# Performance work log

Hardware: AMD Instinct MI355X
Metric: run time of the kernel (lower is better)

The kernel has to match this reference:

```python
import jax, jax.numpy as jnp
import numpy as np

KS = 3          # deformable kernel size
PAD = 1         # padding (kernel_size // 2)
EPS = 1e-5      # BatchNorm eps


def conv2d(x, w, b):
    # plain 3x3 conv, stride 1, pad 1, NCHW / OIHW
    y = jax.lax.conv_general_dilated(x, w, window_strides=(1, 1),
                                     padding=[(PAD, PAD), (PAD, PAD)],
                                     dimension_numbers=("NCHW", "OIHW", "NCHW"))
    return y + b[None, :, None, None]


def deform_conv(x, offset, mask, w, b):
    # modulated deformable conv v2 (torchvision deform_conv2d semantics)
    B, C, H, W = x.shape
    K = KS * KS
    ky, kx = jnp.meshgrid(jnp.arange(KS), jnp.arange(KS), indexing="ij")
    ky = ky.reshape(-1).astype(x.dtype)
    kx = kx.reshape(-1).astype(x.dtype)
    off = offset.reshape(B, K, 2, H, W)          # channel order: (dy, dx) per kernel tap
    dy, dx = off[:, :, 0], off[:, :, 1]          # [B,K,H,W]
    py = dy + (ky - PAD)[None, :, None, None] + jnp.arange(H, dtype=x.dtype)[None, None, :, None]
    px = dx + (kx - PAD)[None, :, None, None] + jnp.arange(W, dtype=x.dtype)[None, None, None, :]
    y0 = jnp.floor(py); x0 = jnp.floor(px)
    ly = py - y0; lx = px - x0
    y0i = y0.astype(jnp.int32); x0i = x0.astype(jnp.int32)
    y1i = y0i + 1; x1i = x0i + 1
    xf = x.reshape(B, C, H * W)

    def gather(yi, xi):
        valid = (yi >= 0) & (yi < H) & (xi >= 0) & (xi < W)          # zero padding outside
        idx = jnp.clip(yi, 0, H - 1) * W + jnp.clip(xi, 0, W - 1)    # [B,K,H,W]
        g = jax.vmap(lambda xb, ib: jnp.take(xb, ib, axis=1))(xf, idx.reshape(B, -1))
        g = g.reshape(B, C, K, H, W)
        return g * valid[:, None].astype(x.dtype)

    v = (gather(y0i, x0i) * ((1 - ly) * (1 - lx))[:, None]
         + gather(y0i, x1i) * ((1 - ly) * lx)[:, None]
         + gather(y1i, x0i) * (ly * (1 - lx))[:, None]
         + gather(y1i, x1i) * (ly * lx)[:, None])                    # [B,C,K,H,W]
    v = v * mask[:, None]                                            # modulation
    out = jnp.einsum("bckhw,ock->bohw", v, w.reshape(w.shape[0], C, K))
    return out + b[None, :, None, None]


def setup_inputs() -> dict:
    key = jax.random.key(0)
    ks = jax.random.split(key, 5)
    B, Cin, Cout, H, W = 8, 64, 64, 128, 128
    K = KS * KS
    x = jax.random.normal(ks[0], (B, Cin, H, W), jnp.float32)
    off_w = jax.random.normal(ks[1], (2 * K, Cin, KS, KS), jnp.float32) * 0.01
    off_b = jnp.zeros((2 * K,), jnp.float32)
    mod_w = jax.random.normal(ks[2], (K, Cin, KS, KS), jnp.float32) * 0.01
    mod_b = jnp.zeros((K,), jnp.float32)
    w = jax.random.normal(ks[3], (Cout, Cin, KS, KS), jnp.float32) * (1.0 / np.sqrt(Cin * K))
    b = jnp.zeros((Cout,), jnp.float32)
    gamma = jnp.ones((Cout,), jnp.float32)
    beta = jnp.zeros((Cout,), jnp.float32)
    return {"x": x, "off_w": off_w, "off_b": off_b, "mod_w": mod_w,
            "mod_b": mod_b, "w": w, "b": b, "gamma": gamma, "beta": beta}


def reference(x, off_w, off_b, mod_w, mod_b, w, b, gamma, beta):
    offset = conv2d(x, off_w, off_b)                       # [B,2K,H,W]
    mask = 2.0 * jax.nn.sigmoid(conv2d(x, mod_w, mod_b))   # [B,K,H,W]
    y = deform_conv(x, offset, mask, w, b)                 # [B,Cout,H,W]
    # BatchNorm2d (training-mode batch stats, biased variance)
    mean = y.mean(axis=(0, 2, 3), keepdims=True)
    var = y.var(axis=(0, 2, 3), keepdims=True)
    yn = (y - mean) / jnp.sqrt(var + EPS)
    yn = gamma[None, :, None, None] * yn + beta[None, :, None, None]
    return jax.nn.relu(yn)
```

## Files before the change

### kernel.cpp

```cpp
#include <hip/hip_runtime.h>
#include <math.h>

#define Hn 128
#define Wn 128
#define HW 16384
#define NPIX 131072
#define EPSv 1e-5f

#define XT_OFF   0
#define WBTA_OFF 4194304
#define WBTB_OFF 4204544
#define STAT_OFF 4225024


typedef short s16x8 __attribute__((ext_vector_type(8)));
typedef unsigned short u16x4 __attribute__((ext_vector_type(4)));
typedef float f32x4 __attribute__((ext_vector_type(4)));
typedef unsigned int u32x4 __attribute__((ext_vector_type(4)));

__device__ __forceinline__ unsigned short f2bf(float f) {
  unsigned u = __float_as_uint(f);
  return (unsigned short)((u + 0x7fffu + ((u >> 16) & 1u)) >> 16);
}
__device__ __forceinline__ float bf2f(unsigned short s) {
  return __uint_as_float((unsigned)s << 16);
}
__device__ __forceinline__ unsigned cvt_pk_bf16(float lo, float hi) {
  unsigned r;
  asm("v_cvt_pk_bf16_f32 %0, %1, %2" : "=v"(r) : "v"(lo), "v"(hi));
  return r;
}

__global__ __launch_bounds__(256) void prep_kernel(
    const float* __restrict__ off_w, const float* __restrict__ mod_w,
    const float* __restrict__ w, unsigned short* __restrict__ wbtA,
    unsigned short* __restrict__ wbtB, float* __restrict__ stat) {
  int i = blockIdx.x * 256 + threadIdx.x;
  if (i < 128) stat[i] = 0.f;
  if (i < 20480) {
    int e = i & 31, oc = (i >> 5) & 31, it = i >> 10;
    int tp = it % 5, chunk = it / 5;
    int tap = tp * 2 + (e >> 4);
    int c = (chunk << 4) + (e & 15);
    float v = 0.f;
    if (tap < 9) {
      if (oc < 18) v = off_w[(oc * 64 + c) * 9 + tap];
      else if (oc < 27) v = mod_w[((oc - 18) * 64 + c) * 9 + tap];
    }
    wbtA[i] = f2bf(v);
  } else if (i < 20480 + 40960) {
    int j = i - 20480;
    int j3 = j & 7;
    int l = (j >> 3) & 63;
    int nt = (j >> 9) & 3;
    int it = j >> 11;
    int tp = it % 5, chunk = it / 5;
    int tap = tp * 2 + (l >> 5);
    int c = (chunk << 4) + (((l >> 4) & 1) << 3) + j3;
    int oc = (nt << 4) + (l & 15);
    float v = (tap < 9) ? w[(oc * 64 + c) * 9 + tap] : 0.f;
    wbtB[j] = f2bf(v);
  }
}

__global__ __launch_bounds__(256) void xform_kernel(
    const float* __restrict__ x, unsigned short* __restrict__ xt) {
  int blk = blockIdx.x;
  int b = blk & 7;
  int hw = ((blk >> 3) << 8) + threadIdx.x;
  const float* xb = x + ((size_t)(b << 6) << 14) + hw;
  unsigned short* o = xt + (((size_t)(b << 14)) + hw) * 64;
#pragma unroll
  for (int g = 0; g < 8; ++g) {
    float v[8];
#pragma unroll
    for (int j = 0; j < 8; ++j) v[j] = xb[(size_t)((g << 3) + j) << 14];
    s16x8 pk;
#pragma unroll
    for (int j = 0; j < 8; ++j) pk[j] = (short)f2bf(v[j]);
    *(s16x8*)(o + (g << 3)) = pk;
  }
}

__global__ __launch_bounds__(256, 4) void fused_dconv_kernel(
    const unsigned short* __restrict__ xt, const unsigned short* __restrict__ wbtA,
    const unsigned short* __restrict__ wbtB,
    const float* __restrict__ off_b, const float* __restrict__ mod_b,
    const float* __restrict__ bias, float* __restrict__ y) {
  __shared__ float offm[27 * 128];
  __shared__ unsigned short geow[9 * 128 * 4];
  __shared__ unsigned short geoi[9 * 128];
  int t = threadIdx.x;
  int bx = blockIdx.x;
  int b = bx & 7, h = bx >> 3;
  int lane = t & 63, wv = t >> 6;
  int ln = lane & 15, quad = (lane >> 4) & 3;
  int hw = h << 7;

  const unsigned short* xtb = xt + ((size_t)(b << 14)) * 64;

  {
    int p0 = (wv << 5) + ln, p1 = p0 + 16;
    int s_ = quad >> 1, cj = (quad & 1) << 3;
    f32x4 acc[2][2];
#pragma unroll
    for (int mt = 0; mt < 2; ++mt)
#pragma unroll
      for (int nt = 0; nt < 2; ++nt) acc[mt][nt] = (f32x4){0.f, 0.f, 0.f, 0.f};

#pragma unroll 5
    for (int it = 0; it < 20; ++it) {
      int chunk = it / 5, tp = it - chunk * 5;
      int tap = tp * 2 + s_;
      s16x8 B0 = (s16x8){0, 0, 0, 0, 0, 0, 0, 0};
      s16x8 B1 = (s16x8){0, 0, 0, 0, 0, 0, 0, 0};
      if (tap < 9) {
        int gy = h + tap / 3 - 1;
        if (gy >= 0 && gy < Hn) {
          const unsigned short* rowp = xtb + ((size_t)(gy << 7)) * 64 + (chunk << 4) + cj;
          int gx0 = p0 + tap % 3 - 1;
          int gx1 = p1 + tap % 3 - 1;
          if (gx0 >= 0 && gx0 < Wn) B0 = *(const s16x8*)(rowp + (gx0 << 6));
          if (gx1 >= 0 && gx1 < Wn) B1 = *(const s16x8*)(rowp + (gx1 << 6));
        }
      }
#pragma unroll
      for (int mt = 0; mt < 2; ++mt) {
        s16x8 A = *(const s16x8*)(wbtA + (size_t)((it << 5) + (mt << 4) + ln) * 32 + (quad << 3));
        acc[mt][0] = __builtin_amdgcn_mfma_f32_16x16x32_bf16(A, B0, acc[mt][0], 0, 0, 0);
        acc[mt][1] = __builtin_amdgcn_mfma_f32_16x16x32_bf16(A, B1, acc[mt][1], 0, 0, 0);
      }
    }

#pragma unroll
    for (int mt = 0; mt < 2; ++mt)
#pragma unroll
      for (int r = 0; r < 4; ++r) {
        int oc = (mt << 4) + (quad << 2) + r;
#pragma unroll
        for (int nt = 0; nt < 2; ++nt) {
          int px = (wv << 5) + (nt << 4) + ln;
          float val = acc[mt][nt][r];
          if (oc < 18) {
            offm[(oc << 7) + px] = val + off_b[oc];
          } else if (oc < 27) {
            float z = val + mod_b[oc - 18];
            offm[(oc << 7) + px] = 2.f / (1.f + expf(-z));
          }
        }
      }
  }
  __syncthreads();

  for (int i = t; i < 1152; i += 256) {
    int tap = i >> 7, p2 = i & 127;
    float dy = offm[((2 * tap) << 7) + p2];
    float dx = offm[((2 * tap + 1) << 7) + p2];
    float m = offm[((18 + tap) << 7) + p2];
    float py = dy + (float)(h + tap / 3 - 1);
    float pxf = dx + (float)(p2 + tap % 3 - 1);
    float y0f = floorf(py), x0f = floorf(pxf);
    float ly = py - y0f, lx = pxf - x0f;
    int y0 = (int)y0f, x0 = (int)x0f;
    int y1 = y0 + 1, x1 = x0 + 1;
    float fy0 = (y0 >= 0 && y0 < Hn) ? 1.f : 0.f;
    float fy1 = (y1 >= 0 && y1 < Hn) ? 1.f : 0.f;
    float fx0 = (x0 >= 0 && x0 < Wn) ? 1.f : 0.f;
    float fx1 = (x1 >= 0 && x1 < Wn) ? 1.f : 0.f;
    float ax0 = (1.f - lx) * fx0, ax1 = lx * fx1;
    float ay0 = (1.f - ly) * fy0 * m, ay1 = ly * fy1 * m;
    int cy0 = min(max(y0, 0), Hn - 1), cy1 = min(max(y1, 0), Hn - 1);
    int cx0 = min(max(x0, 0), Wn - 1), cx1 = min(max(x1, 0), Wn - 1);
    int cbase = min(cx0, Wn - 2), rbase = min(cy0, Hn - 2);
    float gx0 = (cx0 == cbase ? ax0 : 0.f) + (cx1 == cbase ? ax1 : 0.f);
    float gx1 = (cx0 == cbase + 1 ? ax0 : 0.f) + (cx1 == cbase + 1 ? ax1 : 0.f);
    float gy0 = (cy0 == rbase ? ay0 : 0.f) + (cy1 == rbase ? ay1 : 0.f);
    float gy1 = (cy0 == rbase + 1 ? ay0 : 0.f) + (cy1 == rbase + 1 ? ay1 : 0.f);
    unsigned short* gw = geow + i * 4;
    gw[0] = f2bf(gy0 * gx0);
    gw[1] = f2bf(gy0 * gx1);
    gw[2] = f2bf(gy1 * gx0);
    gw[3] = f2bf(gy1 * gx1);
    geoi[i] = (unsigned short)((rbase << 7) + cbase);
  }
  __syncthreads();

  int l4 = ln;
  int s4 = lane >> 4;
  int tapS = lane >> 5;
  int chalf = s4 & 1;

  f32x4 acc[2][4];
#pragma unroll
  for (int m = 0; m < 2; ++m)
#pragma unroll
    for (int n = 0; n < 4; ++n) acc[m][n] = (f32x4){0.f, 0.f, 0.f, 0.f};

  for (int tp = 0; tp < 5; ++tp) {
    int tap = tp * 2 + tapS;
    bool live = (tap < 9);
    float w00[2], w01[2], w10[2], w11[2];
    const unsigned short* cpb[2];
#pragma unroll
    for (int m = 0; m < 2; ++m) {
      if (live) {
        int px = (wv << 5) + (m << 4) + l4;
        int gidx = (tap << 7) + px;
        u16x4 wq = *(const u16x4*)(geow + gidx * 4);
        unsigned ib = geoi[gidx];
        w00[m] = bf2f(wq[0]);
        w01[m] = bf2f(wq[1]);
        w10[m] = bf2f(wq[2]);
        w11[m] = bf2f(wq[3]);
        cpb[m] = xtb + (size_t)ib * 64 + (chalf << 3);
      } else {
        cpb[m] = xtb;
        w00[m] = w01[m] = w10[m] = w11[m] = 0.f;
      }
    }
#pragma unroll 2
    for (int chunk = 0; chunk < 4; ++chunk) {
      int it = chunk * 5 + tp;
      s16x8 A[2];
#pragma unroll
      for (int m = 0; m < 2; ++m) {
        if (live) {
          const unsigned short* cp = cpb[m] + (chunk << 4);
          s16x8 c00 = *(const s16x8*)(cp);
          s16x8 c01 = *(const s16x8*)(cp + 64);
          s16x8 c10 = *(const s16x8*)(cp + 8192);
          s16x8 c11 = *(const s16x8*)(cp + 8192 + 64);
          u32x4 au;
#pragma unroll
          for (int jj = 0; jj < 4; ++jj) {
            float v0 = w00[m] * bf2f((unsigned short)c00[2 * jj]) +
                       w01[m] * bf2f((unsigned short)c01[2 * jj]) +
                       w10[m] * bf2f((unsigned short)c10[2 * jj]) +
                       w11[m] * bf2f((unsigned short)c11[2 * jj]);
            float v1 = w00[m] * bf2f((unsigned short)c00[2 * jj + 1]) +
                       w01[m] * bf2f((unsigned short)c01[2 * jj + 1]) +
                       w10[m] * bf2f((unsigned short)c10[2 * jj + 1]) +
                       w11[m] * bf2f((unsigned short)c11[2 * jj + 1]);
            au[jj] = cvt_pk_bf16(v0, v1);
          }
          A[m] = __builtin_bit_cast(s16x8, au);
        } else {
          A[m] = (s16x8){0, 0, 0, 0, 0, 0, 0, 0};
        }
      }
      const unsigned short* wb = wbtB + (((size_t)it) << 11) + (lane << 3);
#pragma unroll
      for (int n = 0; n < 4; ++n) {
        s16x8 Bf = *(const s16x8*)(wb + (n << 9));
        acc[0][n] = __builtin_amdgcn_mfma_f32_16x16x32_bf16(A[0], Bf, acc[0][n], 0, 0, 0);
        acc[1][n] = __builtin_amdgcn_mfma_f32_16x16x32_bf16(A[1], Bf, acc[1][n], 0, 0, 0);
      }
    }
  }

#pragma unroll
  for (int m = 0; m < 2; ++m) {
    int px0 = (wv << 5) + (m << 4) + (s4 << 2);
#pragma unroll
    for (int n = 0; n < 4; ++n) {
      int oc = (n << 4) + l4;
      float bv = bias[oc];
      float4 o;
      o.x = acc[m][n][0] + bv;
      o.y = acc[m][n][1] + bv;
      o.z = acc[m][n][2] + bv;
      o.w = acc[m][n][3] + bv;
      *(float4*)(y + (((size_t)(b << 6) + oc) << 14) + hw + px0) = o;
    }
  }
}

__global__ __launch_bounds__(256) void stats2_kernel(
    const float* __restrict__ y, float* __restrict__ stat) {
  int bxx = blockIdx.x;
  int c = bxx & 63, sl = bxx >> 6;
  int bb = sl >> 1;
  const float4* yp = (const float4*)(y + (((size_t)bb * 64 + c) << 14) + ((sl & 1) << 13));
  float s = 0.f, ss = 0.f;
  for (int i = threadIdx.x; i < 2048; i += 256) {
    float4 v = yp[i];
    s += v.x + v.y + v.z + v.w;
    ss += v.x * v.x + v.y * v.y + v.z * v.z + v.w * v.w;
  }
#pragma unroll
  for (int o = 32; o > 0; o >>= 1) {
    s += __shfl_xor(s, o);
    ss += __shfl_xor(ss, o);
  }
  __shared__ float shs[4], shss[4];
  int lane = threadIdx.x & 63, wv = threadIdx.x >> 6;
  if (lane == 0) { shs[wv] = s; shss[wv] = ss; }
  __syncthreads();
  if (threadIdx.x == 0) {
    float S = shs[0] + shs[1] + shs[2] + shs[3];
    float SS = shss[0] + shss[1] + shss[2] + shss[3];
    atomicAdd(stat + c, S);
    atomicAdd(stat + 64 + c, SS);
  }
}

__global__ __launch_bounds__(256) void bnrelu_kernel(
    float* __restrict__ y, const float* __restrict__ stat,
    const float* __restrict__ gamma, const float* __restrict__ beta) {
  float4* y4 = (float4*)y;
  for (int i = blockIdx.x * 256 + threadIdx.x; i < 2097152; i += gridDim.x * 256) {
    int c = (i >> 12) & 63;
    float mean = stat[c] * (1.f / (float)NPIX);
    float var = stat[64 + c] * (1.f / (float)NPIX) - mean * mean;
    float r = rsqrtf(var + EPSv);
    float g = gamma[c] * r;
    float bt = beta[c] - mean * g;
    float4 v = y4[i];
    v.x = fmaxf(v.x * g + bt, 0.f);
    v.y = fmaxf(v.y * g + bt, 0.f);
    v.z = fmaxf(v.z * g + bt, 0.f);
    v.w = fmaxf(v.w * g + bt, 0.f);
    y4[i] = v;
  }
}

extern "C" void kernel_launch(void* const* d_in, const int* in_sizes, int n_in,
                              void* d_out, int out_size, void* d_ws, size_t ws_size,
                              hipStream_t stream) {
  const float* x     = (const float*)d_in[0];
  const float* off_w = (const float*)d_in[1];
  const float* off_b = (const float*)d_in[2];
  const float* mod_w = (const float*)d_in[3];
  const float* mod_b = (const float*)d_in[4];
  const float* w     = (const float*)d_in[5];
  const float* b     = (const float*)d_in[6];
  const float* gamma = (const float*)d_in[7];
  const float* beta  = (const float*)d_in[8];
  float* out = (float*)d_out;
  float* ws  = (float*)d_ws;

  unsigned short* xt  = (unsigned short*)(ws + XT_OFF);
  unsigned short* wbtA = (unsigned short*)(ws + WBTA_OFF);
  unsigned short* wbtB = (unsigned short*)(ws + WBTB_OFF);
  float* stat  = ws + STAT_OFF;

  prep_kernel<<<240, 256, 0, stream>>>(off_w, mod_w, w, wbtA, wbtB, stat);
  xform_kernel<<<512, 256, 0, stream>>>(x, xt);
  fused_dconv_kernel<<<1024, 256, 0, stream>>>(xt, wbtA, wbtB, off_b, mod_b, b, out);
  stats2_kernel<<<1024, 256, 0, stream>>>(out, stat);
  bnrelu_kernel<<<8192, 256, 0, stream>>>(out, stat, gamma, beta);
}
```

Before: 230.1 us.

## Fuse BN statistics into deform conv epilogue and batch bilinear gathers per tap

Result: slower. 246.9 us (+7.3%).

```diff
diff --git a/kernel.cpp b/kernel.cpp
--- a/kernel.cpp
+++ b/kernel.cpp
@@ -30,6 +30,9 @@
   asm("v_cvt_pk_bf16_f32 %0, %1, %2" : "=v"(r) : "v"(lo), "v"(hi));
   return r;
 }
+
+#define GLD(dst, ptr, off) \
+  asm volatile("global_load_dwordx4 %0, %1, off offset:" #off : "=&v"(dst) : "v"(ptr))
 
 __global__ __launch_bounds__(256) void prep_kernel(
     const float* __restrict__ off_w, const float* __restrict__ mod_w,
@@ -86,7 +89,8 @@
     const unsigned short* __restrict__ xt, const unsigned short* __restrict__ wbtA,
     const unsigned short* __restrict__ wbtB,
     const float* __restrict__ off_b, const float* __restrict__ mod_b,
-    const float* __restrict__ bias, float* __restrict__ y) {
+    const float* __restrict__ bias, float* __restrict__ y,
+    float* __restrict__ stat) {
   __shared__ float offm[27 * 128];
   __shared__ unsigned short geow[9 * 128 * 4];
   __shared__ unsigned short geoi[9 * 128];
@@ -102,11 +106,11 @@
   {
     int p0 = (wv << 5) + ln, p1 = p0 + 16;
     int s_ = quad >> 1, cj = (quad & 1) << 3;
-    f32x4 acc[2][2];
+    f32x4 acc1[2][2];
 #pragma unroll
     for (int mt = 0; mt < 2; ++mt)
 #pragma unroll
-      for (int nt = 0; nt < 2; ++nt) acc[mt][nt] = (f32x4){0.f, 0.f, 0.f, 0.f};
+      for (int nt = 0; nt < 2; ++nt) acc1[mt][nt] = (f32x4){0.f, 0.f, 0.f, 0.f};
 
 #pragma unroll 5
     for (int it = 0; it < 20; ++it) {
@@ -127,8 +131,8 @@
 #pragma unroll
       for (int mt = 0; mt < 2; ++mt) {
         s16x8 A = *(const s16x8*)(wbtA + (size_t)((it << 5) + (mt << 4) + ln) * 32 + (quad << 3));
-        acc[mt][0] = __builtin_amdgcn_mfma_f32_16x16x32_bf16(A, B0, acc[mt][0], 0, 0, 0);
-        acc[mt][1] = __builtin_amdgcn_mfma_f32_16x16x32_bf16(A, B1, acc[mt][1], 0, 0, 0);
+        acc1[mt][0] = __builtin_amdgcn_mfma_f32_16x16x32_bf16(A, B0, acc1[mt][0], 0, 0, 0);
+        acc1[mt][1] = __builtin_amdgcn_mfma_f32_16x16x32_bf16(A, B1, acc1[mt][1], 0, 0, 0);
       }
     }
 
@@ -140,7 +144,7 @@
 #pragma unroll
         for (int nt = 0; nt < 2; ++nt) {
           int px = (wv << 5) + (nt << 4) + ln;
-          float val = acc[mt][nt][r];
+          float val = acc1[mt][nt][r];
           if (oc < 18) {
             offm[(oc << 7) + px] = val + off_b[oc];
           } else if (oc < 27) {
@@ -196,68 +200,68 @@
 #pragma unroll
     for (int n = 0; n < 4; ++n) acc[m][n] = (f32x4){0.f, 0.f, 0.f, 0.f};
 
-  for (int tp = 0; tp < 5; ++tp) {
-    int tap = tp * 2 + tapS;
-    bool live = (tap < 9);
-    float w00[2], w01[2], w10[2], w11[2];
-    const unsigned short* cpb[2];
-#pragma unroll
-    for (int m = 0; m < 2; ++m) {
-      if (live) {
-        int px = (wv << 5) + (m << 4) + l4;
-        int gidx = (tap << 7) + px;
-        u16x4 wq = *(const u16x4*)(geow + gidx * 4);
-        unsigned ib = geoi[gidx];
-        w00[m] = bf2f(wq[0]);
-        w01[m] = bf2f(wq[1]);
-        w10[m] = bf2f(wq[2]);
-        w11[m] = bf2f(wq[3]);
-        cpb[m] = xtb + (size_t)ib * 64 + (chalf << 3);
-      } else {
-        cpb[m] = xtb;
-        w00[m] = w01[m] = w10[m] = w11[m] = 0.f;
-      }
-    }
-#pragma unroll 2
-    for (int chunk = 0; chunk < 4; ++chunk) {
-      int it = chunk * 5 + tp;
-      s16x8 A[2];
-#pragma unroll
-      for (int m = 0; m < 2; ++m) {
-        if (live) {
-          const unsigned short* cp = cpb[m] + (chunk << 4);
-          s16x8 c00 = *(const s16x8*)(cp);
-          s16x8 c01 = *(const s16x8*)(cp + 64);
-          s16x8 c10 = *(const s16x8*)(cp + 8192);
-          s16x8 c11 = *(const s16x8*)(cp + 8192 + 64);
-          u32x4 au;
-#pragma unroll
-          for (int jj = 0; jj < 4; ++jj) {
-            float v0 = w00[m] * bf2f((unsigned short)c00[2 * jj]) +
-                       w01[m] * bf2f((unsigned short)c01[2 * jj]) +
-                       w10[m] * bf2f((unsigned short)c10[2 * jj]) +
-                       w11[m] * bf2f((unsigned short)c11[2 * jj]);
-            float v1 = w00[m] * bf2f((unsigned short)c00[2 * jj + 1]) +
-                       w01[m] * bf2f((unsigned short)c01[2 * jj + 1]) +
-                       w10[m] * bf2f((unsigned short)c10[2 * jj + 1]) +
-                       w11[m] * bf2f((unsigned short)c11[2 * jj + 1]);
-            au[jj] = cvt_pk_bf16(v0, v1);
-          }
-          A[m] = __builtin_bit_cast(s16x8, au);
-        } else {
-          A[m] = (s16x8){0, 0, 0, 0, 0, 0, 0, 0};
+#pragma unroll
+  for (int m = 0; m < 2; ++m) {
+#pragma unroll 1
+    for (int tp = 0; tp < 5; ++tp) {
+      int tap = tp * 2 + tapS;
+      bool live = (tap < 9);
+      int px = (wv << 5) + (m << 4) + l4;
+      int gidx = ((live ? tap : 0) << 7) + px;
+      u16x4 wq = *(const u16x4*)(geow + gidx * 4);
+      unsigned ib = geoi[gidx];
+      float w00 = live ? bf2f(wq[0]) : 0.f;
+      float w01 = live ? bf2f(wq[1]) : 0.f;
+      float w10 = live ? bf2f(wq[2]) : 0.f;
+      float w11 = live ? bf2f(wq[3]) : 0.f;
+      const unsigned short* base0 = xtb + (size_t)ib * 64 + (chalf << 3);
+      const unsigned short* base1 = base0 + 8192;
+      u32x4 cA0, cA1, cA2, cA3, cB0, cB1, cB2, cB3;
+      u32x4 cC0, cC1, cC2, cC3, cD0, cD1, cD2, cD3;
+      GLD(cA0, base0, 0);   GLD(cA1, base0, 32);  GLD(cA2, base0, 64);  GLD(cA3, base0, 96);
+      GLD(cB0, base0, 128); GLD(cB1, base0, 160); GLD(cB2, base0, 192); GLD(cB3, base0, 224);
+      GLD(cC0, base1, 0);   GLD(cC1, base1, 32);  GLD(cC2, base1, 64);  GLD(cC3, base1, 96);
+      GLD(cD0, base1, 128); GLD(cD1, base1, 160); GLD(cD2, base1, 192); GLD(cD3, base1, 224);
+      asm volatile("s_waitcnt vmcnt(0)" ::: "memory");
+      __builtin_amdgcn_sched_barrier(0);
+      s16x8 c00[4] = {__builtin_bit_cast(s16x8, cA0), __builtin_bit_cast(s16x8, cA1),
+                      __builtin_bit_cast(s16x8, cA2), __builtin_bit_cast(s16x8, cA3)};
+      s16x8 c01[4] = {__builtin_bit_cast(s16x8, cB0), __builtin_bit_cast(s16x8, cB1),
+                      __builtin_bit_cast(s16x8, cB2), __builtin_bit_cast(s16x8, cB3)};
+      s16x8 c10[4] = {__builtin_bit_cast(s16x8, cC0), __builtin_bit_cast(s16x8, cC1),
+                      __builtin_bit_cast(s16x8, cC2), __builtin_bit_cast(s16x8, cC3)};
+      s16x8 c11[4] = {__builtin_bit_cast(s16x8, cD0), __builtin_bit_cast(s16x8, cD1),
+                      __builtin_bit_cast(s16x8, cD2), __builtin_bit_cast(s16x8, cD3)};
+#pragma unroll
+      for (int chunk = 0; chunk < 4; ++chunk) {
+        int it = chunk * 5 + tp;
+        u32x4 au;
+#pragma unroll
+        for (int jj = 0; jj < 4; ++jj) {
+          float v0 = w00 * bf2f((unsigned short)c00[chunk][2 * jj]) +
+                     w01 * bf2f((unsigned short)c01[chunk][2 * jj]) +
+                     w10 * bf2f((unsigned short)c10[chunk][2 * jj]) +
+                     w11 * bf2f((unsigned short)c11[chunk][2 * jj]);
+          float v1 = w00 * bf2f((unsigned short)c00[chunk][2 * jj + 1]) +
+                     w01 * bf2f((unsigned short)c01[chunk][2 * jj + 1]) +
+                     w10 * bf2f((unsigned short)c10[chunk][2 * jj + 1]) +
+                     w11 * bf2f((unsigned short)c11[chunk][2 * jj + 1]);
+          au[jj] = cvt_pk_bf16(v0, v1);
+        }
+        s16x8 A = __builtin_bit_cast(s16x8, au);
+        const unsigned short* wb = wbtB + (((size_t)it) << 11) + (lane << 3);
+#pragma unroll
+        for (int n = 0; n < 4; ++n) {
+          s16x8 Bf = *(const s16x8*)(wb + (n << 9));
+          acc[m][n] = __builtin_amdgcn_mfma_f32_16x16x32_bf16(A, Bf, acc[m][n], 0, 0, 0);
         }
       }
-      const unsigned short* wb = wbtB + (((size_t)it) << 11) + (lane << 3);
-#pragma unroll
-      for (int n = 0; n < 4; ++n) {
-        s16x8 Bf = *(const s16x8*)(wb + (n << 9));
-        acc[0][n] = __builtin_amdgcn_mfma_f32_16x16x32_bf16(A[0], Bf, acc[0][n], 0, 0, 0);
-        acc[1][n] = __builtin_amdgcn_mfma_f32_16x16x32_bf16(A[1], Bf, acc[1][n], 0, 0, 0);
-      }
-    }
-  }
-
+    }
+  }
+
+  float sac[4], ssc[4];
+#pragma unroll
+  for (int n = 0; n < 4; ++n) { sac[n] = 0.f; ssc[n] = 0.f; }
 #pragma unroll
   for (int m = 0; m < 2; ++m) {
     int px0 = (wv << 5) + (m << 4) + (s4 << 2);
@@ -270,37 +274,32 @@
       o.y = acc[m][n][1] + bv;
       o.z = acc[m][n][2] + bv;
       o.w = acc[m][n][3] + bv;
+      sac[n] += o.x + o.y + o.z + o.w;
+      ssc[n] += o.x * o.x + o.y * o.y + o.z * o.z + o.w * o.w;
       *(float4*)(y + (((size_t)(b << 6) + oc) << 14) + hw + px0) = o;
     }
   }
-}
-
-__global__ __launch_bounds__(256) void stats2_kernel(
-    const float* __restrict__ y, float* __restrict__ stat) {
-  int bxx = blockIdx.x;
-  int c = bxx & 63, sl = bxx >> 6;
-  int bb = sl >> 1;
-  const float4* yp = (const float4*)(y + (((size_t)bb * 64 + c) << 14) + ((sl & 1) << 13));
-  float s = 0.f, ss = 0.f;
-  for (int i = threadIdx.x; i < 2048; i += 256) {
-    float4 v = yp[i];
-    s += v.x + v.y + v.z + v.w;
-    ss += v.x * v.x + v.y * v.y + v.z * v.z + v.w * v.w;
-  }
-#pragma unroll
-  for (int o = 32; o > 0; o >>= 1) {
-    s += __shfl_xor(s, o);
-    ss += __shfl_xor(ss, o);
-  }
-  __shared__ float shs[4], shss[4];
-  int lane = threadIdx.x & 63, wv = threadIdx.x >> 6;
-  if (lane == 0) { shs[wv] = s; shss[wv] = ss; }
+#pragma unroll
+  for (int n = 0; n < 4; ++n) {
+    sac[n] += __shfl_xor(sac[n], 16);
+    sac[n] += __shfl_xor(sac[n], 32);
+    ssc[n] += __shfl_xor(ssc[n], 16);
+    ssc[n] += __shfl_xor(ssc[n], 32);
+  }
+  if (lane < 16) {
+#pragma unroll
+    for (int n = 0; n < 4; ++n) {
+      int oc = (n << 4) + lane;
+      offm[(wv << 6) + oc] = sac[n];
+      offm[256 + (wv << 6) + oc] = ssc[n];
+    }
+  }
   __syncthreads();
-  if (threadIdx.x == 0) {
-    float S = shs[0] + shs[1] + shs[2] + shs[3];
-    float SS = shss[0] + shss[1] + shss[2] + shss[3];
-    atomicAdd(stat + c, S);
-    atomicAdd(stat + 64 + c, SS);
+  if (t < 64) {
+    float S = offm[t] + offm[64 + t] + offm[128 + t] + offm[192 + t];
+    float SS = offm[256 + t] + offm[320 + t] + offm[384 + t] + offm[448 + t];
+    atomicAdd(stat + t, S);
+    atomicAdd(stat + 64 + t, SS);
   }
 }
 
@@ -346,7 +345,6 @@
 
   prep_kernel<<<240, 256, 0, stream>>>(off_w, mod_w, w, wbtA, wbtB, stat);
   xform_kernel<<<512, 256, 0, stream>>>(x, xt);
-  fused_dconv_kernel<<<1024, 256, 0, stream>>>(xt, wbtA, wbtB, off_b, mod_b, b, out);
-  stats2_kernel<<<1024, 256, 0, stream>>>(out, stat);
+  fused_dconv_kernel<<<1024, 256, 0, stream>>>(xt, wbtA, wbtB, off_b, mod_b, b, out, stat);
   bnrelu_kernel<<<8192, 256, 0, stream>>>(out, stat, gamma, beta);
 }
```
